# Performance work log

Hardware: AMD Instinct MI355X
Metric: run time of the kernel (lower is better)

The kernel has to match this reference:

```python
import jax, jax.numpy as jnp
import numpy as np

KEY_DIM = 1024
VALUE_DIM = 1024
NUM_HEADS = 16
ORIGIN_SHAPE = (8, 16, 16)  # T, H, W video-token grid
LOCAL_BLOCKS = 3
B = 1
S = int(np.prod(ORIGIN_SHAPE))  # 2048
DH = KEY_DIM // NUM_HEADS       # 64
DV = VALUE_DIM // NUM_HEADS


def make_layout():
    """Vectorized equivalent of SparseAttention.make_layout (causal=True)."""
    shape = np.array(ORIGIN_SHAPE, dtype=np.int64)
    cum = np.concatenate([np.flip(np.cumprod(np.flip(shape)))[1:], [1]]).astype(np.int64)
    idx = np.arange(S, dtype=np.int64)
    coords = (idx[None, :] // cum[:, None]) % shape[:, None]  # [ndim, S]
    diff = idx[:, None] - idx[None, :]
    layout = (diff >= 0) & (diff <= LOCAL_BLOCKS)  # causal local window
    for d in range(len(ORIGIN_SHAPE) - 1):  # causal axial strides along dims 0..ndim-2
        same = np.ones((S, S), dtype=bool)
        for e in range(len(ORIGIN_SHAPE)):
            if e != d:
                same &= coords[e][:, None] == coords[e][None, :]
        layout |= same & (coords[d][None, :] <= coords[d][:, None])
    return layout  # [S, S] bool


def setup_inputs() -> dict:
    key = jax.random.key(0)
    ks = jax.random.split(key, 11)
    sc = 0.02
    inp = {
        "query": jax.random.normal(ks[0], (B, S, KEY_DIM), jnp.float32),
        "key":   jax.random.normal(ks[1], (B, S, KEY_DIM), jnp.float32),
        "value": jax.random.normal(ks[2], (B, S, VALUE_DIM), jnp.float32),
        "wq": sc * jax.random.normal(ks[3], (KEY_DIM, KEY_DIM), jnp.float32),
        "bq": jnp.zeros((KEY_DIM,), jnp.float32),
        "wk": sc * jax.random.normal(ks[4], (KEY_DIM, KEY_DIM), jnp.float32),
        "bk": jnp.zeros((KEY_DIM,), jnp.float32),
        "wv": sc * jax.random.normal(ks[5], (VALUE_DIM, VALUE_DIM), jnp.float32),
        "bv": jnp.zeros((VALUE_DIM,), jnp.float32),
        "wo": sc * jax.random.normal(ks[6], (VALUE_DIM, KEY_DIM), jnp.float32),
        "bo": jnp.zeros((KEY_DIM,), jnp.float32),
        "layout": jnp.asarray(make_layout(), jnp.int32)[None, None],  # [1,1,S,S]
    }
    return inp


def reference(query, key, value, wq, bq, wk, bk, wv, bv, wo, bo, layout):
    def split(x, d):  # [B,S,H*d] -> [B,H,S,d]
        return x.reshape(B, S, NUM_HEADS, d).transpose(0, 2, 1, 3)
    q = split(query @ wq + bq, DH)
    k = split(key @ wk + bk, DH)
    v = split(value @ wv + bv, DV)
    logits = jnp.einsum('bhsd,bhtd->bhst', q, k) / jnp.sqrt(jnp.float32(DH))
    logits = jnp.where(layout > 0, logits, jnp.float32(-1e9))
    attn = jax.nn.softmax(logits, axis=-1)  # matches tf.sparse.softmax over layout support
    out = jnp.einsum('bhst,bhtd->bhsd', attn, v)
    out = out.transpose(0, 2, 1, 3).reshape(B, S, VALUE_DIM)
    return out @ wo + bo
```

## Files before the change

kernel.cpp:

```cpp
#include <hip/hip_runtime.h>
#include <hip/hip_bf16.h>
#include <cstdint>
#include <math.h>

#define SEQ    2048
#define DMODEL 1024
#define NHEAD  16
#define DHEAD  64
#define NZPAD  32

typedef __bf16 bf16;
typedef __bf16 bf16x8 __attribute__((ext_vector_type(8)));
typedef float  f32x4  __attribute__((ext_vector_type(4)));

typedef __attribute__((address_space(3))) uint32_t lds_u32;
typedef __attribute__((address_space(1))) const uint32_t global_u32;

__device__ __forceinline__ void async_load16(const void* g, void* l) {
    __builtin_amdgcn_global_load_lds((global_u32*)g, (lds_u32*)l, 16, 0, 0);
}

#define CAST_BLOCKS 3072
#define TR_BLOCKS   4096
#define NZ_BLOCKS   512

__global__ __launch_bounds__(256) void prep_kernel(
    const float* __restrict__ q, const float* __restrict__ k, const float* __restrict__ v,
    bf16* __restrict__ qx, bf16* __restrict__ kx, bf16* __restrict__ vx,
    const float* __restrict__ w0, const float* __restrict__ w1,
    const float* __restrict__ w2, const float* __restrict__ w3,
    bf16* __restrict__ t0, bf16* __restrict__ t1,
    bf16* __restrict__ t2, bf16* __restrict__ t3,
    const int* __restrict__ layout, int* __restrict__ nzidx, int* __restrict__ nzcnt) {
    __shared__ float tile[32][33];
    const int bid = blockIdx.x;
    if (bid < CAST_BLOCKS) {
        const int z = bid >> 10;
        const float* src = (z == 0) ? q : (z == 1) ? k : v;
        bf16* dst        = (z == 0) ? qx : (z == 1) ? kx : vx;
        const int i = (bid & 1023) * 256 + threadIdx.x;
        const float4* s4 = (const float4*)src;
        float4 a = s4[i * 2 + 0];
        float4 b = s4[i * 2 + 1];
        bf16x8 o;
        o[0] = (bf16)a.x; o[1] = (bf16)a.y; o[2] = (bf16)a.z; o[3] = (bf16)a.w;
        o[4] = (bf16)b.x; o[5] = (bf16)b.y; o[6] = (bf16)b.z; o[7] = (bf16)b.w;
        ((bf16x8*)dst)[i] = o;
    } else if (bid < CAST_BLOCKS + TR_BLOCKS) {
        const int b = bid - CAST_BLOCKS;
        const int z = b >> 10, rem = b & 1023;
        const float* w = (z == 0) ? w0 : (z == 1) ? w1 : (z == 2) ? w2 : w3;
        bf16* t        = (z == 0) ? t0 : (z == 1) ? t1 : (z == 2) ? t2 : t3;
        const int tx = threadIdx.x & 31, ty = threadIdx.x >> 5;
        const int kbase = (rem >> 5) * 32, nbase = (rem & 31) * 32;
#pragma unroll
        for (int i = 0; i < 4; ++i)
            tile[ty + 8 * i][tx] = w[(size_t)(kbase + ty + 8 * i) * DMODEL + nbase + tx];
        __syncthreads();
#pragma unroll
        for (int i = 0; i < 4; ++i)
            t[(size_t)(nbase + ty + 8 * i) * DMODEL + kbase + tx] = (bf16)tile[tx][ty + 8 * i];
    } else {
        const int b = bid - CAST_BLOCKS - TR_BLOCKS;
        const int wv = threadIdx.x >> 6, lane = threadIdx.x & 63;
        const int s = b * 4 + wv;
        const int* row = layout + (size_t)s * SEQ;
        int base = 0;
        for (int it = 0; it < SEQ / 64; ++it) {
            const int col = it * 64 + lane;
            const bool nz = row[col] > 0;
            const unsigned long long mask = __ballot(nz);
            if (nz) {
                const int pos = base + __popcll(mask & ((1ull << lane) - 1ull));
                if (pos < NZPAD) nzidx[s * NZPAD + pos] = col;
            }
            base += __popcll(mask);
        }
        const int cnt = (base < NZPAD) ? base : NZPAD;
        if (lane >= cnt && lane < NZPAD) nzidx[s * NZPAD + lane] = s;
        if (lane == 0) nzcnt[s] = cnt;
    }
}

template <typename OutT>
__device__ __forceinline__ void gemm_bt_body(
    const bf16* __restrict__ A, const bf16* __restrict__ BT,
    const float* __restrict__ bias, OutT* __restrict__ C) {
    constexpr int K = 1024, N = 1024;
    __shared__ bf16 sA[128 * 32];
    __shared__ bf16 sB[128 * 32];
    const int tid = threadIdx.x;
    const int w = tid >> 6, lane = tid & 63;
    const int wm = w >> 1, wn = w & 1;
    const int lr = lane & 15, quad = lane >> 4;
    const int m0 = blockIdx.y * 128, n0 = blockIdx.x * 128;

    f32x4 acc[4][4] = {};
    float bia[4];
#pragma unroll
    for (int ni = 0; ni < 4; ++ni) bia[ni] = bias[n0 + wn * 64 + ni * 16 + lr];

    for (int kt = 0; kt < K; kt += 32) {
#pragma unroll
        for (int r = 0; r < 2; ++r) {
            const int c = r * 256 + w * 64 + lane;
            const int row = c >> 2, ch = c & 3;
            const bf16* ga = A + (size_t)(m0 + row) * K + kt + ch * 8;
            const bf16* gb = BT + (size_t)(n0 + row) * K + kt + ch * 8;
            char* la = (char*)sA + (r * 256 + w * 64) * 16;
            char* lb = (char*)sB + (r * 256 + w * 64) * 16;
            async_load16(ga, la);
            async_load16(gb, lb);
        }
        __syncthreads();

        bf16x8 af[4], bfr[4];
#pragma unroll
        for (int mi = 0; mi < 4; ++mi)
            af[mi] = *(const bf16x8*)&sA[(wm * 64 + mi * 16 + lr) * 32 + quad * 8];
#pragma unroll
        for (int ni = 0; ni < 4; ++ni)
            bfr[ni] = *(const bf16x8*)&sB[(wn * 64 + ni * 16 + lr) * 32 + quad * 8];
#pragma unroll
        for (int mi = 0; mi < 4; ++mi)
#pragma unroll
            for (int ni = 0; ni < 4; ++ni)
                acc[mi][ni] = __builtin_amdgcn_mfma_f32_16x16x32_bf16(
                    af[mi], bfr[ni], acc[mi][ni], 0, 0, 0);
        __syncthreads();
    }

#pragma unroll
    for (int mi = 0; mi < 4; ++mi)
#pragma unroll
        for (int ni = 0; ni < 4; ++ni) {
            const int row = m0 + wm * 64 + mi * 16 + quad * 4;
            const int col = n0 + wn * 64 + ni * 16 + lr;
            const f32x4 vv = acc[mi][ni];
#pragma unroll
            for (int r = 0; r < 4; ++r)
                C[(size_t)(row + r) * N + col] = (OutT)(vv[r] + bia[ni]);
        }
}

__global__ __launch_bounds__(256) void proj3_kernel(
    const bf16* qx, const bf16* kx, const bf16* vx,
    const bf16* wqT, const bf16* wkT, const bf16* wvT,
    const float* bq, const float* bk, const float* bv,
    bf16* qp, bf16* kp, bf16* vp) {
    const int z = blockIdx.z;
    const bf16* A  = (z == 0) ? qx : (z == 1) ? kx : vx;
    const bf16* BT = (z == 0) ? wqT : (z == 1) ? wkT : wvT;
    const float* b = (z == 0) ? bq : (z == 1) ? bk : bv;
    bf16* C        = (z == 0) ? qp : (z == 1) ? kp : vp;
    gemm_bt_body<bf16>(A, BT, b, C);
}

__global__ __launch_bounds__(256) void gemm_final_kernel(
    const bf16* A, const bf16* BT, const float* bias, float* C) {
    gemm_bt_body<float>(A, BT, bias, C);
}

__global__ __launch_bounds__(256) void attn_kernel(
    const bf16* __restrict__ qp, const bf16* __restrict__ kp, const bf16* __restrict__ vp,
    const int* __restrict__ nzidx, const int* __restrict__ nzcnt,
    bf16* __restrict__ ao) {
    const int wv = threadIdx.x >> 6, lane = threadIdx.x & 63;
    const int p = blockIdx.x * 4 + wv;
    const int s = __builtin_amdgcn_readfirstlane(p & (SEQ - 1));
    const int h = __builtin_amdgcn_readfirstlane(p >> 11);
    const int hoff = h * DHEAD + lane;

    const float q = (float)qp[(size_t)s * DMODEL + hoff];
    const int cnt = nzcnt[s];
    const int* idx = nzidx + s * NZPAD;
    int t[NZPAD];
#pragma unroll
    for (int c = 0; c < NZPAD; ++c) t[c] = idx[c];

    float pr[NZPAD];
#pragma unroll
    for (int c = 0; c < NZPAD; ++c)
        pr[c] = q * (float)kp[(size_t)t[c] * DMODEL + hoff];

#pragma unroll
    for (int step = 0; step < 5; ++step) {
        const int mask = 1 << step;
        const int half = NZPAD >> (step + 1);
        const bool hi = (lane & mask) != 0;
#pragma unroll
        for (int c = 0; c < half; ++c) {
            const float a = pr[2 * c], b = pr[2 * c + 1];
            const float mine = hi ? b : a;
            const float oth  = hi ? a : b;
            pr[c] = mine + __shfl_xor(oth, mask);
        }
    }
    const float dotv = pr[0] + __shfl_xor(pr[0], 32);

    const int c_lane = lane & 31;
    const float logit = (c_lane < cnt) ? dotv * 0.125f : -1e30f;
    float m = logit;
    m = fmaxf(m, __shfl_xor(m, 1)); m = fmaxf(m, __shfl_xor(m, 2));
    m = fmaxf(m, __shfl_xor(m, 4)); m = fmaxf(m, __shfl_xor(m, 8));
    m = fmaxf(m, __shfl_xor(m, 16));
    const float e = __expf(logit - m);
    float ssum = e;
    ssum += __shfl_xor(ssum, 1); ssum += __shfl_xor(ssum, 2);
    ssum += __shfl_xor(ssum, 4); ssum += __shfl_xor(ssum, 8);
    ssum += __shfl_xor(ssum, 16);
    const float prob = e / ssum;

    float acc = 0.f;
#pragma unroll
    for (int c = 0; c < NZPAD; ++c)
        acc += __shfl(prob, c) * (float)vp[(size_t)t[c] * DMODEL + hoff];
    ao[(size_t)s * DMODEL + hoff] = (bf16)acc;
}

extern "C" void kernel_launch(void* const* d_in, const int* in_sizes, int n_in,
                              void* d_out, int out_size, void* d_ws, size_t ws_size,
                              hipStream_t stream) {
    const float* query = (const float*)d_in[0];
    const float* key   = (const float*)d_in[1];
    const float* value = (const float*)d_in[2];
    const float* wq = (const float*)d_in[3];
    const float* bq = (const float*)d_in[4];
    const float* wk = (const float*)d_in[5];
    const float* bk = (const float*)d_in[6];
    const float* wv = (const float*)d_in[7];
    const float* bv = (const float*)d_in[8];
    const float* wo = (const float*)d_in[9];
    const float* bo = (const float*)d_in[10];
    const int* layout = (const int*)d_in[11];
    float* out = (float*)d_out;

    char* ws = (char*)d_ws;
    auto alloc = [&](size_t bytes) {
        char* p = ws;
        ws += (bytes + 255) & ~(size_t)255;
        return p;
    };
    bf16* qx  = (bf16*)alloc((size_t)SEQ * DMODEL * 2);
    bf16* kx  = (bf16*)alloc((size_t)SEQ * DMODEL * 2);
    bf16* vx  = (bf16*)alloc((size_t)SEQ * DMODEL * 2);
    bf16* wqT = (bf16*)alloc((size_t)DMODEL * DMODEL * 2);
    bf16* wkT = (bf16*)alloc((size_t)DMODEL * DMODEL * 2);
    bf16* wvT = (bf16*)alloc((size_t)DMODEL * DMODEL * 2);
    bf16* woT = (bf16*)alloc((size_t)DMODEL * DMODEL * 2);
    bf16* qp  = (bf16*)alloc((size_t)SEQ * DMODEL * 2);
    bf16* kp  = (bf16*)alloc((size_t)SEQ * DMODEL * 2);
    bf16* vp  = (bf16*)alloc((size_t)SEQ * DMODEL * 2);
    bf16* ao  = (bf16*)alloc((size_t)SEQ * DMODEL * 2);
    int* nzidx = (int*)alloc((size_t)SEQ * NZPAD * 4);
    int* nzcnt = (int*)alloc((size_t)SEQ * 4);

    prep_kernel<<<dim3(CAST_BLOCKS + TR_BLOCKS + NZ_BLOCKS), 256, 0, stream>>>(
        query, key, value, qx, kx, vx,
        wq, wk, wv, wo, wqT, wkT, wvT, woT,
        layout, nzidx, nzcnt);
    proj3_kernel<<<dim3(8, 16, 3), 256, 0, stream>>>(
        qx, kx, vx, wqT, wkT, wvT, bq, bk, bv, qp, kp, vp);
    attn_kernel<<<dim3(NHEAD * SEQ / 4), 256, 0, stream>>>(qp, kp, vp, nzidx, nzcnt, ao);
    gemm_final_kernel<<<dim3(8, 16), 256, 0, stream>>>(ao, woT, bo, out);
}
```

Before: 192.1 us.

## Halve GEMM M-tile for more blocks and restructure sparse attention dot products

The projection and output GEMMs take a template M-tile, now 64 rows, and the grid doubles in y so more workgroups cover the 256 CUs. The attention kernel now assigns one nonzero key per lane half. Each lane loads 32 contiguous bf16 q/k elements as vectors and computes the partial dot directly, replacing 32 scalar gathers and a 5-stage shuffle-transpose reduction. V values are prefetched before the softmax, and probabilities are broadcast with readlane instead of shfl, at the cost of more registers and more B-tile reloads in the GEMMs.

```diff
diff --git a/kernel.cpp b/kernel.cpp
--- a/kernel.cpp
+++ b/kernel.cpp
@@ -82,47 +82,52 @@
     }
 }
 
-template <typename OutT>
+template <int TM, typename OutT>
 __device__ __forceinline__ void gemm_bt_body(
     const bf16* __restrict__ A, const bf16* __restrict__ BT,
     const float* __restrict__ bias, OutT* __restrict__ C) {
     constexpr int K = 1024, N = 1024;
-    __shared__ bf16 sA[128 * 32];
+    constexpr int MI  = TM / 32;
+    constexpr int ACH = TM * 4;
+    __shared__ bf16 sA[TM * 32];
     __shared__ bf16 sB[128 * 32];
     const int tid = threadIdx.x;
     const int w = tid >> 6, lane = tid & 63;
     const int wm = w >> 1, wn = w & 1;
     const int lr = lane & 15, quad = lane >> 4;
-    const int m0 = blockIdx.y * 128, n0 = blockIdx.x * 128;
-
-    f32x4 acc[4][4] = {};
+    const int m0 = blockIdx.y * TM, n0 = blockIdx.x * 128;
+
+    f32x4 acc[MI][4] = {};
     float bia[4];
 #pragma unroll
     for (int ni = 0; ni < 4; ++ni) bia[ni] = bias[n0 + wn * 64 + ni * 16 + lr];
 
     for (int kt = 0; kt < K; kt += 32) {
 #pragma unroll
-        for (int r = 0; r < 2; ++r) {
-            const int c = r * 256 + w * 64 + lane;
-            const int row = c >> 2, ch = c & 3;
-            const bf16* ga = A + (size_t)(m0 + row) * K + kt + ch * 8;
-            const bf16* gb = BT + (size_t)(n0 + row) * K + kt + ch * 8;
-            char* la = (char*)sA + (r * 256 + w * 64) * 16;
-            char* lb = (char*)sB + (r * 256 + w * 64) * 16;
-            async_load16(ga, la);
-            async_load16(gb, lb);
+        for (int kk = 0; kk < (ACH + 512) / 256; ++kk) {
+            const int cb = kk * 256 + w * 64;
+            const int c  = cb + lane;
+            if (cb < ACH) {
+                const int row = c >> 2, ch = c & 3;
+                async_load16(A + (size_t)(m0 + row) * K + kt + ch * 8,
+                             (char*)sA + cb * 16);
+            } else {
+                const int c2 = c - ACH, row = c2 >> 2, ch = c2 & 3;
+                async_load16(BT + (size_t)(n0 + row) * K + kt + ch * 8,
+                             (char*)sB + (cb - ACH) * 16);
+            }
         }
         __syncthreads();
 
-        bf16x8 af[4], bfr[4];
-#pragma unroll
-        for (int mi = 0; mi < 4; ++mi)
-            af[mi] = *(const bf16x8*)&sA[(wm * 64 + mi * 16 + lr) * 32 + quad * 8];
+        bf16x8 af[MI], bfr[4];
+#pragma unroll
+        for (int mi = 0; mi < MI; ++mi)
+            af[mi] = *(const bf16x8*)&sA[(wm * (TM / 2) + mi * 16 + lr) * 32 + quad * 8];
 #pragma unroll
         for (int ni = 0; ni < 4; ++ni)
             bfr[ni] = *(const bf16x8*)&sB[(wn * 64 + ni * 16 + lr) * 32 + quad * 8];
 #pragma unroll
-        for (int mi = 0; mi < 4; ++mi)
+        for (int mi = 0; mi < MI; ++mi)
 #pragma unroll
             for (int ni = 0; ni < 4; ++ni)
                 acc[mi][ni] = __builtin_amdgcn_mfma_f32_16x16x32_bf16(
@@ -131,10 +136,10 @@
     }
 
 #pragma unroll
-    for (int mi = 0; mi < 4; ++mi)
+    for (int mi = 0; mi < MI; ++mi)
 #pragma unroll
         for (int ni = 0; ni < 4; ++ni) {
-            const int row = m0 + wm * 64 + mi * 16 + quad * 4;
+            const int row = m0 + wm * (TM / 2) + mi * 16 + quad * 4;
             const int col = n0 + wn * 64 + ni * 16 + lr;
             const f32x4 vv = acc[mi][ni];
 #pragma unroll
@@ -153,12 +158,12 @@
     const bf16* BT = (z == 0) ? wqT : (z == 1) ? wkT : wvT;
     const float* b = (z == 0) ? bq : (z == 1) ? bk : bv;
     bf16* C        = (z == 0) ? qp : (z == 1) ? kp : vp;
-    gemm_bt_body<bf16>(A, BT, b, C);
+    gemm_bt_body<64, bf16>(A, BT, b, C);
 }
 
 __global__ __launch_bounds__(256) void gemm_final_kernel(
     const bf16* A, const bf16* BT, const float* bias, float* C) {
-    gemm_bt_body<float>(A, BT, bias, C);
+    gemm_bt_body<64, float>(A, BT, bias, C);
 }
 
 __global__ __launch_bounds__(256) void attn_kernel(
@@ -169,37 +174,39 @@
     const int p = blockIdx.x * 4 + wv;
     const int s = __builtin_amdgcn_readfirstlane(p & (SEQ - 1));
     const int h = __builtin_amdgcn_readfirstlane(p >> 11);
-    const int hoff = h * DHEAD + lane;
-
-    const float q = (float)qp[(size_t)s * DMODEL + hoff];
+    const int hbase = h * DHEAD;
+    const int hoff = hbase + lane;
+
     const int cnt = nzcnt[s];
     const int* idx = nzidx + s * NZPAD;
     int t[NZPAD];
 #pragma unroll
     for (int c = 0; c < NZPAD; ++c) t[c] = idx[c];
 
-    float pr[NZPAD];
+    const int c_lane = lane & 31;
+    const int fo = (lane >> 5) << 5;
+    const int myT = idx[c_lane];
+
+    const bf16x8* qrow = (const bf16x8*)(qp + (size_t)s * DMODEL + hbase + fo);
+    const bf16x8* krow = (const bf16x8*)(kp + (size_t)myT * DMODEL + hbase + fo);
+    bf16x8 qc[4], kc[4];
+#pragma unroll
+    for (int j = 0; j < 4; ++j) { qc[j] = qrow[j]; kc[j] = krow[j]; }
+
+    float vvv[NZPAD];
 #pragma unroll
     for (int c = 0; c < NZPAD; ++c)
-        pr[c] = q * (float)kp[(size_t)t[c] * DMODEL + hoff];
-
-#pragma unroll
-    for (int step = 0; step < 5; ++step) {
-        const int mask = 1 << step;
-        const int half = NZPAD >> (step + 1);
-        const bool hi = (lane & mask) != 0;
-#pragma unroll
-        for (int c = 0; c < half; ++c) {
-            const float a = pr[2 * c], b = pr[2 * c + 1];
-            const float mine = hi ? b : a;
-            const float oth  = hi ? a : b;
-            pr[c] = mine + __shfl_xor(oth, mask);
-        }
-    }
-    const float dotv = pr[0] + __shfl_xor(pr[0], 32);
-
-    const int c_lane = lane & 31;
-    const float logit = (c_lane < cnt) ? dotv * 0.125f : -1e30f;
+        vvv[c] = (float)vp[(size_t)t[c] * DMODEL + hoff];
+
+    float dot = 0.f;
+#pragma unroll
+    for (int j = 0; j < 4; ++j)
+#pragma unroll
+        for (int e = 0; e < 8; ++e)
+            dot = fmaf((float)qc[j][e], (float)kc[j][e], dot);
+    dot += __shfl_xor(dot, 32);
+
+    const float logit = (c_lane < cnt) ? dot * 0.125f : -1e30f;
     float m = logit;
     m = fmaxf(m, __shfl_xor(m, 1)); m = fmaxf(m, __shfl_xor(m, 2));
     m = fmaxf(m, __shfl_xor(m, 4)); m = fmaxf(m, __shfl_xor(m, 8));
@@ -213,8 +220,11 @@
 
     float acc = 0.f;
 #pragma unroll
-    for (int c = 0; c < NZPAD; ++c)
-        acc += __shfl(prob, c) * (float)vp[(size_t)t[c] * DMODEL + hoff];
+    for (int c = 0; c < NZPAD; ++c) {
+        const float pc = __uint_as_float(
+            __builtin_amdgcn_readlane(__float_as_uint(prob), c));
+        acc = fmaf(pc, vvv[c], acc);
+    }
     ao[(size_t)s * DMODEL + hoff] = (bf16)acc;
 }
 
@@ -259,8 +269,8 @@
         query, key, value, qx, kx, vx,
         wq, wk, wv, wo, wqT, wkT, wvT, woT,
         layout, nzidx, nzcnt);
-    proj3_kernel<<<dim3(8, 16, 3), 256, 0, stream>>>(
+    proj3_kernel<<<dim3(8, 32, 3), 256, 0, stream>>>(
         qx, kx, vx, wqT, wkT, wvT, bq, bk, bv, qp, kp, vp);
     attn_kernel<<<dim3(NHEAD * SEQ / 4), 256, 0, stream>>>(qp, kp, vp, nzidx, nzcnt, ao);
-    gemm_final_kernel<<<dim3(8, 16), 256, 0, stream>>>(ao, woT, bo, out);
-}
+    gemm_final_kernel<<<dim3(8, 32), 256, 0, stream>>>(ao, woT, bo, out);
+}
```

Result: faster. 184.9 us (-3.7%).
